# Optimization experiments

Hardware: AMD Instinct MI355X
Metric: run time of the kernel (lower is better)

Reference implementation:

```python
import jax, jax.numpy as jnp
import numpy as np

N_NODES = 50000
N_RAND_EDGES = 800000
N_GRAPHS = 64
IN_DIM, HID, HEADS = 1024, 64, 4
NEG_SLOPE = 0.2  # PyG GATConv default


def setup_inputs() -> dict:
    key = jax.random.key(0)
    ks = jax.random.split(key, 16)
    x = jax.random.normal(ks[0], (N_NODES, IN_DIM), dtype=jnp.float32)
    src = jax.random.randint(ks[1], (N_RAND_EDGES,), 0, N_NODES, dtype=jnp.int32)
    dst = jax.random.randint(ks[2], (N_RAND_EDGES,), 0, N_NODES, dtype=jnp.int32)
    loop = jnp.arange(N_NODES, dtype=jnp.int32)
    # PyG GATConv adds self-loops by default; bake them into edge_index.
    edge_index = jnp.stack([jnp.concatenate([src, loop]), jnp.concatenate([dst, loop])])
    batch = jnp.sort(jax.random.randint(ks[3], (N_NODES,), 0, N_GRAPHS, dtype=jnp.int32))
    s = 0.05
    W1 = jax.random.normal(ks[4], (IN_DIM, HEADS * HID), dtype=jnp.float32) * s
    att_src1 = jax.random.normal(ks[5], (HEADS, HID), dtype=jnp.float32) * s
    att_dst1 = jax.random.normal(ks[6], (HEADS, HID), dtype=jnp.float32) * s
    b1 = jnp.zeros((HEADS * HID,), dtype=jnp.float32)
    W2 = jax.random.normal(ks[7], (HEADS * HID, HID), dtype=jnp.float32) * s
    att_src2 = jax.random.normal(ks[8], (1, HID), dtype=jnp.float32) * s
    att_dst2 = jax.random.normal(ks[9], (1, HID), dtype=jnp.float32) * s
    b2 = jnp.zeros((HID,), dtype=jnp.float32)
    fc_w = jax.random.normal(ks[10], (HID, 2), dtype=jnp.float32) * s
    fc_b = jnp.zeros((2,), dtype=jnp.float32)
    return {"x": x, "edge_index": edge_index, "batch": batch,
            "W1": W1, "att_src1": att_src1, "att_dst1": att_dst1, "b1": b1,
            "W2": W2, "att_src2": att_src2, "att_dst2": att_dst2, "b2": b2,
            "fc_w": fc_w, "fc_b": fc_b}


def gat_conv(x, src, dst, W, a_src, a_dst, b):
    """PyG GATConv (eval mode, concat=True). x:[N,Fin] -> [N, H*C]."""
    N = x.shape[0]
    H, C = a_src.shape
    h = (x @ W).reshape(N, H, C)                      # [N,H,C]
    al_s = jnp.einsum('nhc,hc->nh', h, a_src)         # [N,H]
    al_d = jnp.einsum('nhc,hc->nh', h, a_dst)
    e = jax.nn.leaky_relu(al_s[src] + al_d[dst], NEG_SLOPE)   # [E,H]
    # segment-softmax over edges grouped by destination node
    m = jax.ops.segment_max(e, dst, num_segments=N)           # [N,H]
    w = jnp.exp(e - m[dst])
    denom = jax.ops.segment_sum(w, dst, num_segments=N)
    alpha = w / denom[dst]                                    # [E,H]
    msg = h[src] * alpha[:, :, None]                          # [E,H,C]
    out = jax.ops.segment_sum(msg, dst, num_segments=N)       # [N,H,C]
    return out.reshape(N, H * C) + b


def reference(x, edge_index, batch, W1, att_src1, att_dst1, b1,
              W2, att_src2, att_dst2, b2, fc_w, fc_b):
    src, dst = edge_index[0], edge_index[1]
    # dropout is identity in eval mode
    h = jax.nn.elu(gat_conv(x, src, dst, W1, att_src1, att_dst1, b1))
    h = jax.nn.elu(gat_conv(h, src, dst, W2, att_src2, att_dst2, b2))
    # global mean pool over graphs
    sums = jax.ops.segment_sum(h, batch, num_segments=N_GRAPHS)          # [G,HID]
    cnt = jax.ops.segment_sum(jnp.ones((h.shape[0],), h.dtype), batch,
                              num_segments=N_GRAPHS)
    pooled = sums / jnp.maximum(cnt, 1.0)[:, None]
    return pooled @ fc_w + fc_b                                          # [G,2]
```

## Files before the change

kernel.cpp:

```cpp
#include <hip/hip_runtime.h>
#include <hip/hip_bf16.h>

#define NNODES   50000
#define NGRAPHS  64
#define INDIM    1024
#define HIDC     64
#define HEADS1   4
#define F1       (HEADS1*HIDC)
#define NEG_SLOPE 0.2f

#define WS_COUNTS   0
#define WS_ZEROLEN  50000
#define WS_INDPTR   54208
#define WS_CURSOR   104256
#define WS_CSRSRC   154304
#define WS_CSRDST   1004304
#define WS_BSUM     1854304
#define WS_ALS1     1854368
#define WS_ALD1     2054368
#define WS_ALS2     2254368
#define WS_ALD2     2304368
#define WS_BP       2354368
#define WS_BP2      2485440
#define WS_H1B      2493632
#define WS_X2B      8893632
#define WS_H2B      15293632
#define WS_HFIN     16893632

typedef __attribute__((ext_vector_type(8))) short bf16x8;
typedef __attribute__((ext_vector_type(4))) float f32x4;

__device__ __forceinline__ ushort f2bf(float f) {
    union { float f; uint u; } v; v.f = f;
    uint r = v.u + 0x7fff + ((v.u >> 16) & 1);
    return (ushort)(r >> 16);
}
__device__ __forceinline__ float bf2f(ushort u) {
    union { uint u; float f; } v; v.u = (uint)u << 16; return v.f;
}

__global__ void zero_kernel(float* p, int n) {
    int i = blockIdx.x * blockDim.x + threadIdx.x;
    if (i < n) p[i] = 0.0f;
}

__global__ void hist_kernel(const int* __restrict__ dst, int* __restrict__ counts, int E) {
    int i = blockIdx.x * blockDim.x + threadIdx.x;
    if (i < E) atomicAdd(&counts[dst[i]], 1);
}

__global__ __launch_bounds__(1024) void scan1_kernel(const int* __restrict__ counts,
                                                     int* __restrict__ indptr,
                                                     int* __restrict__ bsum, int N) {
    __shared__ int sm[1024];
    int b = blockIdx.x;
    int i = b * 1024 + (int)threadIdx.x;
    int v = (i < N) ? counts[i] : 0;
    sm[threadIdx.x] = v;
    __syncthreads();
    for (int off = 1; off < 1024; off <<= 1) {
        int t = (threadIdx.x >= (unsigned)off) ? sm[threadIdx.x - off] : 0;
        __syncthreads();
        sm[threadIdx.x] += t;
        __syncthreads();
    }
    if (i < N) indptr[i + 1] = sm[threadIdx.x];
    if (threadIdx.x == 1023) bsum[b] = sm[1023];
}

__global__ void scan2_kernel(int* __restrict__ bsum, int nb) {
    int lane = threadIdx.x;
    int v = (lane < nb) ? bsum[lane] : 0;
    int orig = v;
    #pragma unroll
    for (int off = 1; off < 64; off <<= 1) {
        int t = __shfl_up(v, off, 64);
        if (lane >= off) v += t;
    }
    if (lane < nb) bsum[lane] = v - orig;
}

__global__ __launch_bounds__(1024) void scan3_kernel(const int* __restrict__ counts,
                                                     int* __restrict__ indptr,
                                                     int* __restrict__ cursor,
                                                     const int* __restrict__ bsum, int N) {
    int i = blockIdx.x * 1024 + (int)threadIdx.x;
    if (i == 0) indptr[0] = 0;
    if (i < N) {
        int incl = indptr[i + 1] + bsum[blockIdx.x];
        indptr[i + 1] = incl;
        cursor[i] = incl - counts[i];
    }
}

__global__ void fill_kernel(const int* __restrict__ src, const int* __restrict__ dst,
                            int* __restrict__ cursor, int* __restrict__ csr_src,
                            int* __restrict__ csr_dst, int E) {
    int i = blockIdx.x * blockDim.x + threadIdx.x;
    if (i < E) {
        int d = dst[i];
        int pos = atomicAdd(&cursor[d], 1);
        csr_src[pos] = src[i];
        csr_dst[pos] = d;
    }
}

__global__ void pack_w1(const float* __restrict__ W, ushort* __restrict__ Bp) {
    int o = blockIdx.x * blockDim.x + threadIdx.x;
    int j = o & 7;
    int lane = (o >> 3) & 63;
    int kchunk = (o >> 9) & 31;
    int ntile = o >> 14;
    int k = kchunk * 32 + (lane >> 4) * 8 + j;
    int n = ntile * 16 + (lane & 15);
    Bp[o] = f2bf(W[k * 256 + n]);
}

__global__ void pack_w2(const float* __restrict__ W, ushort* __restrict__ Bp) {
    int o = blockIdx.x * blockDim.x + threadIdx.x;
    int j = o & 7;
    int lane = (o >> 3) & 63;
    int kchunk = (o >> 9) & 7;
    int ntile = o >> 12;
    int k = kchunk * 32 + (lane >> 4) * 8 + j;
    int n = ntile * 16 + (lane & 15);
    Bp[o] = f2bf(W[k * 64 + n]);
}

__global__ __launch_bounds__(256) void gemm1_mfma(const float* __restrict__ A,
                                                  const ushort* __restrict__ Bp,
                                                  ushort* __restrict__ C,
                                                  const float* __restrict__ asrc,
                                                  const float* __restrict__ adst,
                                                  float* __restrict__ als,
                                                  float* __restrict__ ald,
                                                  int M) {
    __shared__ __align__(16) ushort Atile[2][128 * 32];
    const int K = 1024, N = 256;
    int tid = threadIdx.x;
    int lane = tid & 63;
    int w = tid >> 6;
    int wm = w >> 1, wn = w & 1;
    int m0 = blockIdx.x * 128;

    const float* srow[4];
    int soff[4];
    #pragma unroll
    for (int l = 0; l < 4; ++l) {
        int slot = l * 256 + tid;
        int m = slot >> 3, hc = slot & 7;
        int c = hc >> 1;
        int row = m0 + m; if (row >= M) row = M - 1;
        srow[l] = A + (size_t)row * K + hc * 4;
        soff[l] = (m * 4 + (c ^ ((m >> 1) & 3))) * 8 + (hc & 1) * 4;
    }
    int afrag_off[4];
    #pragma unroll
    for (int mt = 0; mt < 4; ++mt) {
        int r = wm * 64 + mt * 16 + (lane & 15);
        int cq = lane >> 4;
        afrag_off[mt] = (r * 4 + (cq ^ ((r >> 1) & 3))) * 8;
    }
    const ushort* bbase[8];
    #pragma unroll
    for (int nt = 0; nt < 8; ++nt) {
        int ntile = wn * 8 + nt;
        bbase[nt] = Bp + ((size_t)(ntile * 32) * 64 + lane) * 8;
    }

    f32x4 acc[4][8] = {};
    float4 v[4];
    #pragma unroll
    for (int l = 0; l < 4; ++l) v[l] = *(const float4*)(srow[l]);

    for (int kc = 0; kc < 32; ++kc) {
        ushort* At = Atile[kc & 1];
        #pragma unroll
        for (int l = 0; l < 4; ++l) {
            ushort4 b;
            b.x = f2bf(v[l].x); b.y = f2bf(v[l].y);
            b.z = f2bf(v[l].z); b.w = f2bf(v[l].w);
            *(ushort4*)&At[soff[l]] = b;
        }
        __syncthreads();
        if (kc < 31) {
            #pragma unroll
            for (int l = 0; l < 4; ++l)
                v[l] = *(const float4*)(srow[l] + (kc + 1) * 32);
        }
        bf16x8 afr[4];
        #pragma unroll
        for (int mt = 0; mt < 4; ++mt)
            afr[mt] = *(const bf16x8*)&At[afrag_off[mt]];
        #pragma unroll
        for (int nt = 0; nt < 8; ++nt) {
            bf16x8 bfr = *(const bf16x8*)(bbase[nt] + (size_t)kc * 64 * 8);
            #pragma unroll
            for (int mt = 0; mt < 4; ++mt)
                acc[mt][nt] = __builtin_amdgcn_mfma_f32_16x16x32_bf16(afr[mt], bfr, acc[mt][nt], 0, 0, 0);
        }
    }

    float a_s[8], a_d[8];
    #pragma unroll
    for (int nt = 0; nt < 8; ++nt) {
        int col = wn * 128 + nt * 16 + (lane & 15);
        a_s[nt] = asrc[col];
        a_d[nt] = adst[col];
    }
    #pragma unroll
    for (int mt = 0; mt < 4; ++mt) {
        #pragma unroll
        for (int nt = 0; nt < 8; ++nt) {
            int col = wn * 128 + nt * 16 + (lane & 15);
            #pragma unroll
            for (int r = 0; r < 4; ++r) {
                int row = m0 + wm * 64 + mt * 16 + (lane >> 4) * 4 + r;
                if (row < M) C[(size_t)row * N + col] = f2bf(acc[mt][nt][r]);
            }
        }
        #pragma unroll
        for (int hg = 0; hg < 2; ++hg) {
            int head = wn * 2 + hg;
            #pragma unroll
            for (int r = 0; r < 4; ++r) {
                int row = m0 + wm * 64 + mt * 16 + (lane >> 4) * 4 + r;
                float s = 0.f, d = 0.f;
                #pragma unroll
                for (int q = 0; q < 4; ++q) {
                    float c = acc[mt][4 * hg + q][r];
                    s = fmaf(c, a_s[4 * hg + q], s);
                    d = fmaf(c, a_d[4 * hg + q], d);
                }
                #pragma unroll
                for (int off = 1; off < 16; off <<= 1) {
                    s += __shfl_xor(s, off, 64);
                    d += __shfl_xor(d, off, 64);
                }
                if ((lane & 15) == 0 && row < M) {
                    als[row * 4 + head] = s;
                    ald[row * 4 + head] = d;
                }
            }
        }
    }
}

__global__ __launch_bounds__(256) void gemm2_mfma(const ushort* __restrict__ Ab,
                                                  const ushort* __restrict__ Bp,
                                                  ushort* __restrict__ C,
                                                  const float* __restrict__ asrc,
                                                  const float* __restrict__ adst,
                                                  float* __restrict__ als,
                                                  float* __restrict__ ald,
                                                  int M) {
    int tid = threadIdx.x;
    int lane = tid & 63;
    int w = tid >> 6;
    int m0 = blockIdx.x * 128 + w * 32;

    f32x4 acc[2][4] = {};
    #pragma unroll 2
    for (int kc = 0; kc < 8; ++kc) {
        bf16x8 afr[2];
        #pragma unroll
        for (int mt = 0; mt < 2; ++mt) {
            int r = m0 + mt * 16 + (lane & 15);
            if (r >= M) r = M - 1;
            afr[mt] = *(const bf16x8*)&Ab[(size_t)r * 256 + kc * 32 + (lane >> 4) * 8];
        }
        #pragma unroll
        for (int nt = 0; nt < 4; ++nt) {
            bf16x8 bfr = *(const bf16x8*)&Bp[((nt * 8 + kc) * 64 + lane) * 8];
            acc[0][nt] = __builtin_amdgcn_mfma_f32_16x16x32_bf16(afr[0], bfr, acc[0][nt], 0, 0, 0);
            acc[1][nt] = __builtin_amdgcn_mfma_f32_16x16x32_bf16(afr[1], bfr, acc[1][nt], 0, 0, 0);
        }
    }
    float a_s[4], a_d[4];
    #pragma unroll
    for (int nt = 0; nt < 4; ++nt) {
        a_s[nt] = asrc[nt * 16 + (lane & 15)];
        a_d[nt] = adst[nt * 16 + (lane & 15)];
    }
    #pragma unroll
    for (int mt = 0; mt < 2; ++mt) {
        #pragma unroll
        for (int nt = 0; nt < 4; ++nt) {
            int col = nt * 16 + (lane & 15);
            #pragma unroll
            for (int r = 0; r < 4; ++r) {
                int row = m0 + mt * 16 + (lane >> 4) * 4 + r;
                if (row < M) C[(size_t)row * 64 + col] = f2bf(acc[mt][nt][r]);
            }
        }
        #pragma unroll
        for (int r = 0; r < 4; ++r) {
            int row = m0 + mt * 16 + (lane >> 4) * 4 + r;
            float s = 0.f, d = 0.f;
            #pragma unroll
            for (int nt = 0; nt < 4; ++nt) {
                float c = acc[mt][nt][r];
                s = fmaf(c, a_s[nt], s);
                d = fmaf(c, a_d[nt], d);
            }
            #pragma unroll
            for (int off = 1; off < 16; off <<= 1) {
                s += __shfl_xor(s, off, 64);
                d += __shfl_xor(d, off, 64);
            }
            if ((lane & 15) == 0 && row < M) {
                als[row] = s;
                ald[row] = d;
            }
        }
    }
}

__device__ __forceinline__ float wave_reduce_sum(float v) {
    #pragma unroll
    for (int off = 32; off > 0; off >>= 1) v += __shfl_xor(v, off, 64);
    return v;
}

__device__ __forceinline__ float edge_w(float e) {
    e = (e > 0.f) ? e : NEG_SLOPE * e;
    return __expf(e);
}

__global__ __launch_bounds__(256) void agg1_kernel(const ushort* __restrict__ h,
                                                   const float* __restrict__ als,
                                                   const float* __restrict__ ald,
                                                   const int* __restrict__ indptr,
                                                   const int* __restrict__ csr_src,
                                                   const float* __restrict__ bias,
                                                   ushort* __restrict__ out, int N) {
    __shared__ float4 lacc[4][64];
    __shared__ float  lden[4][64];
    int n = blockIdx.x;
    int lane = threadIdx.x & 63;
    int wv = threadIdx.x >> 6;
    int hd = lane >> 4;
    int beg = indptr[n], end = indptr[n + 1];
    float ald_h = ald[n * 4 + hd];
    float4 acc = make_float4(0.f, 0.f, 0.f, 0.f);
    float den = 0.f;
    int p = beg + wv;
    for (; p + 4 < end; p += 8) {
        int s0 = csr_src[p], s1 = csr_src[p + 4];
        float w0 = edge_w(als[s0 * 4 + hd] + ald_h);
        float w1 = edge_w(als[s1 * 4 + hd] + ald_h);
        ushort4 a0 = *(const ushort4*)&h[(size_t)s0 * 256 + lane * 4];
        ushort4 a1 = *(const ushort4*)&h[(size_t)s1 * 256 + lane * 4];
        acc.x = fmaf(w0, bf2f(a0.x), fmaf(w1, bf2f(a1.x), acc.x));
        acc.y = fmaf(w0, bf2f(a0.y), fmaf(w1, bf2f(a1.y), acc.y));
        acc.z = fmaf(w0, bf2f(a0.z), fmaf(w1, bf2f(a1.z), acc.z));
        acc.w = fmaf(w0, bf2f(a0.w), fmaf(w1, bf2f(a1.w), acc.w));
        den += w0 + w1;
    }
    if (p < end) {
        int s0 = csr_src[p];
        float w0 = edge_w(als[s0 * 4 + hd] + ald_h);
        ushort4 a0 = *(const ushort4*)&h[(size_t)s0 * 256 + lane * 4];
        acc.x = fmaf(w0, bf2f(a0.x), acc.x);
        acc.y = fmaf(w0, bf2f(a0.y), acc.y);
        acc.z = fmaf(w0, bf2f(a0.z), acc.z);
        acc.w = fmaf(w0, bf2f(a0.w), acc.w);
        den += w0;
    }
    lacc[wv][lane] = acc;
    lden[wv][lane] = den;
    __syncthreads();
    if (wv == 0) {
        float4 a = lacc[0][lane];
        float4 a1 = lacc[1][lane], a2 = lacc[2][lane], a3 = lacc[3][lane];
        a.x += a1.x + a2.x + a3.x;
        a.y += a1.y + a2.y + a3.y;
        a.z += a1.z + a2.z + a3.z;
        a.w += a1.w + a2.w + a3.w;
        float d = lden[0][lane] + lden[1][lane] + lden[2][lane] + lden[3][lane];
        float4 bv = *(const float4*)&bias[lane * 4];
        float inv = 1.0f / d;
        float o0 = a.x * inv + bv.x, o1 = a.y * inv + bv.y;
        float o2 = a.z * inv + bv.z, o3 = a.w * inv + bv.w;
        o0 = (o0 > 0.f) ? o0 : (__expf(o0) - 1.0f);
        o1 = (o1 > 0.f) ? o1 : (__expf(o1) - 1.0f);
        o2 = (o2 > 0.f) ? o2 : (__expf(o2) - 1.0f);
        o3 = (o3 > 0.f) ? o3 : (__expf(o3) - 1.0f);
        ushort4 ob; ob.x = f2bf(o0); ob.y = f2bf(o1); ob.z = f2bf(o2); ob.w = f2bf(o3);
        *(ushort4*)&out[(size_t)n * 256 + lane * 4] = ob;
    }
}

__global__ __launch_bounds__(256) void agg2_kernel(const ushort* __restrict__ h,
                                                   const float* __restrict__ als,
                                                   const float* __restrict__ ald,
                                                   const int* __restrict__ indptr,
                                                   const int* __restrict__ csr_src,
                                                   const float* __restrict__ bias,
                                                   float* __restrict__ out, int N) {
    __shared__ float2 lacc[8][32];
    __shared__ float  lden[8][32];
    int n = blockIdx.x;
    int lane = threadIdx.x & 63;
    int wv = threadIdx.x >> 6;
    int sl = wv * 2 + (lane >> 5);
    int l32 = lane & 31;
    int beg = indptr[n], end = indptr[n + 1];
    float ald_n = ald[n];
    float2 acc = make_float2(0.f, 0.f);
    float den = 0.f;
    for (int p = beg + sl; p < end; p += 8) {
        int s = csr_src[p];
        float wt = edge_w(als[s] + ald_n);
        ushort2 hv = *(const ushort2*)&h[(size_t)s * 64 + l32 * 2];
        acc.x = fmaf(wt, bf2f(hv.x), acc.x);
        acc.y = fmaf(wt, bf2f(hv.y), acc.y);
        den += wt;
    }
    lacc[sl][l32] = acc;
    lden[sl][l32] = den;
    __syncthreads();
    if (threadIdx.x < 32) {
        int c = threadIdx.x;
        float2 a = make_float2(0.f, 0.f);
        float d = 0.f;
        #pragma unroll
        for (int s = 0; s < 8; ++s) {
            a.x += lacc[s][c].x; a.y += lacc[s][c].y;
            d += lden[s][c];
        }
        float inv = 1.0f / d;
        float o0 = a.x * inv + bias[c * 2];
        float o1 = a.y * inv + bias[c * 2 + 1];
        o0 = (o0 > 0.f) ? o0 : (__expf(o0) - 1.0f);
        o1 = (o1 > 0.f) ? o1 : (__expf(o1) - 1.0f);
        *(float2*)&out[(size_t)n * 64 + c * 2] = make_float2(o0, o1);
    }
}

__global__ __launch_bounds__(256) void pool_fc_kernel(const float* __restrict__ hfin,
                                                      const int* __restrict__ batch,
                                                      const float* __restrict__ fc_w,
                                                      const float* __restrict__ fc_b,
                                                      float* __restrict__ out, int N) {
    __shared__ float lacc[4][64];
    int g = blockIdx.x;
    int beg, end;
    {
        int lo = 0, hi = N;
        while (lo < hi) { int mid = (lo + hi) >> 1; if (batch[mid] < g) lo = mid + 1; else hi = mid; }
        beg = lo;
        lo = beg; hi = N;
        while (lo < hi) { int mid = (lo + hi) >> 1; if (batch[mid] < g + 1) lo = mid + 1; else hi = mid; }
        end = lo;
    }
    int lane = threadIdx.x & 63;
    int wv = threadIdx.x >> 6;
    float acc = 0.f;
    for (int n = beg + wv; n < end; n += 4)
        acc += hfin[(size_t)n * 64 + lane];
    lacc[wv][lane] = acc;
    __syncthreads();
    if (wv == 0) {
        float s = lacc[0][lane] + lacc[1][lane] + lacc[2][lane] + lacc[3][lane];
        float cnt = fmaxf((float)(end - beg), 1.0f);
        float pooled = s / cnt;
        float p0 = wave_reduce_sum(pooled * fc_w[lane * 2 + 0]);
        float p1 = wave_reduce_sum(pooled * fc_w[lane * 2 + 1]);
        if (lane == 0) {
            out[g * 2 + 0] = p0 + fc_b[0];
            out[g * 2 + 1] = p1 + fc_b[1];
        }
    }
}

extern "C" void kernel_launch(void* const* d_in, const int* in_sizes, int n_in,
                              void* d_out, int out_size, void* d_ws, size_t ws_size,
                              hipStream_t stream) {
    const float* x      = (const float*)d_in[0];
    const int*   ei     = (const int*)d_in[1];
    const int*   batch  = (const int*)d_in[2];
    const float* W1     = (const float*)d_in[3];
    const float* asrc1  = (const float*)d_in[4];
    const float* adst1  = (const float*)d_in[5];
    const float* b1     = (const float*)d_in[6];
    const float* W2     = (const float*)d_in[7];
    const float* asrc2  = (const float*)d_in[8];
    const float* adst2  = (const float*)d_in[9];
    const float* b2     = (const float*)d_in[10];
    const float* fc_w   = (const float*)d_in[11];
    const float* fc_b   = (const float*)d_in[12];
    float* out          = (float*)d_out;

    const int N = in_sizes[2];
    const int E = in_sizes[1] / 2;
    const int* src = ei;
    const int* dst = ei + E;

    float* ws = (float*)d_ws;
    int*    counts  = (int*)(ws + WS_COUNTS);
    int*    indptr  = (int*)(ws + WS_INDPTR);
    int*    cursor  = (int*)(ws + WS_CURSOR);
    int*    csr_src = (int*)(ws + WS_CSRSRC);
    int*    csr_dst = (int*)(ws + WS_CSRDST);
    int*    bsum    = (int*)(ws + WS_BSUM);
    float*  al_s1   = ws + WS_ALS1;
    float*  al_d1   = ws + WS_ALD1;
    float*  al_s2   = ws + WS_ALS2;
    float*  al_d2   = ws + WS_ALD2;
    ushort* bp      = (ushort*)(ws + WS_BP);
    ushort* bp2     = (ushort*)(ws + WS_BP2);
    ushort* h1b     = (ushort*)(ws + WS_H1B);
    ushort* x2b     = (ushort*)(ws + WS_X2B);
    ushort* h2b     = (ushort*)(ws + WS_H2B);
    float*  hfin    = ws + WS_HFIN;

    const int nb = (N + 1023) / 1024;

    zero_kernel<<<(WS_ZEROLEN + 255) / 256, 256, 0, stream>>>(ws, WS_ZEROLEN);
    pack_w1<<<(INDIM * F1) / 256, 256, 0, stream>>>(W1, bp);
    pack_w2<<<(F1 * HIDC) / 256, 256, 0, stream>>>(W2, bp2);
    hist_kernel<<<(E + 255) / 256, 256, 0, stream>>>(dst, counts, E);
    scan1_kernel<<<nb, 1024, 0, stream>>>(counts, indptr, bsum, N);
    scan2_kernel<<<1, 64, 0, stream>>>(bsum, nb);
    scan3_kernel<<<nb, 1024, 0, stream>>>(counts, indptr, cursor, bsum, N);
    fill_kernel<<<(E + 255) / 256, 256, 0, stream>>>(src, dst, cursor, csr_src, csr_dst, E);
    gemm1_mfma<<<(N + 127) / 128, 256, 0, stream>>>(
        x, bp, h1b, asrc1, adst1, al_s1, al_d1, N);
    agg1_kernel<<<N, 256, 0, stream>>>(h1b, al_s1, al_d1, indptr, csr_src, b1, x2b, N);
    gemm2_mfma<<<(N + 127) / 128, 256, 0, stream>>>(
        x2b, bp2, h2b, asrc2, adst2, al_s2, al_d2, N);
    agg2_kernel<<<N, 256, 0, stream>>>(h2b, al_s2, al_d2, indptr, csr_src, b2, hfin, N);
    pool_fc_kernel<<<NGRAPHS, 256, 0, stream>>>(hfin, batch, fc_w, fc_b, out, N);
}
```

Measured before the change: 638.5 us.

## Assign one wave per node in aggregation with LDS-staged edge weights; fuse prep kernels

The aggregation kernels now give each destination node to a single wave (agg1) or half-wave (agg2) instead of a whole block. This removes the cross-wave LDS reduction and __syncthreads, and cuts the grid from N blocks to N/4 and N/8. Each wave loads up to 64 (or 32) edge sources cooperatively, computes the per-head softmax weights once, and stages them in LDS so the gather loop does not recompute exp per lane. The zeroing and the two weight-packing kernels are merged into one launch, and the unused csr_dst write in fill_kernel is dropped. The trade-off is less parallelism per node for high-degree nodes and a serial per-wave edge loop.

Measured after the change: 575.9 us. -9.8%, faster.

```diff
diff --git a/kernel.cpp b/kernel.cpp
--- a/kernel.cpp
+++ b/kernel.cpp
@@ -39,9 +39,33 @@
     union { uint u; float f; } v; v.u = (uint)u << 16; return v.f;
 }
 
-__global__ void zero_kernel(float* p, int n) {
-    int i = blockIdx.x * blockDim.x + threadIdx.x;
-    if (i < n) p[i] = 0.0f;
+__global__ void prep_kernel(const float* __restrict__ W1, const float* __restrict__ W2,
+                            ushort* __restrict__ Bp1, ushort* __restrict__ Bp2,
+                            int* __restrict__ counts) {
+    int b = blockIdx.x;
+    int tid = threadIdx.x;
+    if (b < 1024) {
+        int o = b * 256 + tid;
+        int j = o & 7;
+        int lane = (o >> 3) & 63;
+        int kchunk = (o >> 9) & 31;
+        int ntile = o >> 14;
+        int k = kchunk * 32 + (lane >> 4) * 8 + j;
+        int n = ntile * 16 + (lane & 15);
+        Bp1[o] = f2bf(W1[k * 256 + n]);
+    } else if (b < 1088) {
+        int o = (b - 1024) * 256 + tid;
+        int j = o & 7;
+        int lane = (o >> 3) & 63;
+        int kchunk = (o >> 9) & 7;
+        int ntile = o >> 12;
+        int k = kchunk * 32 + (lane >> 4) * 8 + j;
+        int n = ntile * 16 + (lane & 15);
+        Bp2[o] = f2bf(W2[k * 64 + n]);
+    } else {
+        int i = (b - 1088) * 256 + tid;
+        if (i < NNODES) counts[i] = 0;
+    }
 }
 
 __global__ void hist_kernel(const int* __restrict__ dst, int* __restrict__ counts, int E) {
@@ -94,37 +118,13 @@
 }
 
 __global__ void fill_kernel(const int* __restrict__ src, const int* __restrict__ dst,
-                            int* __restrict__ cursor, int* __restrict__ csr_src,
-                            int* __restrict__ csr_dst, int E) {
+                            int* __restrict__ cursor, int* __restrict__ csr_src, int E) {
     int i = blockIdx.x * blockDim.x + threadIdx.x;
     if (i < E) {
         int d = dst[i];
         int pos = atomicAdd(&cursor[d], 1);
         csr_src[pos] = src[i];
-        csr_dst[pos] = d;
-    }
-}
-
-__global__ void pack_w1(const float* __restrict__ W, ushort* __restrict__ Bp) {
-    int o = blockIdx.x * blockDim.x + threadIdx.x;
-    int j = o & 7;
-    int lane = (o >> 3) & 63;
-    int kchunk = (o >> 9) & 31;
-    int ntile = o >> 14;
-    int k = kchunk * 32 + (lane >> 4) * 8 + j;
-    int n = ntile * 16 + (lane & 15);
-    Bp[o] = f2bf(W[k * 256 + n]);
-}
-
-__global__ void pack_w2(const float* __restrict__ W, ushort* __restrict__ Bp) {
-    int o = blockIdx.x * blockDim.x + threadIdx.x;
-    int j = o & 7;
-    int lane = (o >> 3) & 63;
-    int kchunk = (o >> 9) & 7;
-    int ntile = o >> 12;
-    int k = kchunk * 32 + (lane >> 4) * 8 + j;
-    int n = ntile * 16 + (lane & 15);
-    Bp[o] = f2bf(W[k * 64 + n]);
+    }
 }
 
 __global__ __launch_bounds__(256) void gemm1_mfma(const float* __restrict__ A,
@@ -334,61 +334,53 @@
                                                    const int* __restrict__ csr_src,
                                                    const float* __restrict__ bias,
                                                    ushort* __restrict__ out, int N) {
-    __shared__ float4 lacc[4][64];
-    __shared__ float  lden[4][64];
-    int n = blockIdx.x;
+    __shared__ int   s_s[4][64];
+    __shared__ float s_w[4][64][4];
+    int wv   = threadIdx.x >> 6;
     int lane = threadIdx.x & 63;
-    int wv = threadIdx.x >> 6;
+    int n = blockIdx.x * 4 + wv;
+    if (n >= N) return;
     int hd = lane >> 4;
     int beg = indptr[n], end = indptr[n + 1];
-    float ald_h = ald[n * 4 + hd];
+    float4 aldv = *(const float4*)&ald[n * 4];
+
     float4 acc = make_float4(0.f, 0.f, 0.f, 0.f);
     float den = 0.f;
-    int p = beg + wv;
-    for (; p + 4 < end; p += 8) {
-        int s0 = csr_src[p], s1 = csr_src[p + 4];
-        float w0 = edge_w(als[s0 * 4 + hd] + ald_h);
-        float w1 = edge_w(als[s1 * 4 + hd] + ald_h);
-        ushort4 a0 = *(const ushort4*)&h[(size_t)s0 * 256 + lane * 4];
-        ushort4 a1 = *(const ushort4*)&h[(size_t)s1 * 256 + lane * 4];
-        acc.x = fmaf(w0, bf2f(a0.x), fmaf(w1, bf2f(a1.x), acc.x));
-        acc.y = fmaf(w0, bf2f(a0.y), fmaf(w1, bf2f(a1.y), acc.y));
-        acc.z = fmaf(w0, bf2f(a0.z), fmaf(w1, bf2f(a1.z), acc.z));
-        acc.w = fmaf(w0, bf2f(a0.w), fmaf(w1, bf2f(a1.w), acc.w));
-        den += w0 + w1;
-    }
-    if (p < end) {
-        int s0 = csr_src[p];
-        float w0 = edge_w(als[s0 * 4 + hd] + ald_h);
-        ushort4 a0 = *(const ushort4*)&h[(size_t)s0 * 256 + lane * 4];
-        acc.x = fmaf(w0, bf2f(a0.x), acc.x);
-        acc.y = fmaf(w0, bf2f(a0.y), acc.y);
-        acc.z = fmaf(w0, bf2f(a0.z), acc.z);
-        acc.w = fmaf(w0, bf2f(a0.w), acc.w);
-        den += w0;
-    }
-    lacc[wv][lane] = acc;
-    lden[wv][lane] = den;
-    __syncthreads();
-    if (wv == 0) {
-        float4 a = lacc[0][lane];
-        float4 a1 = lacc[1][lane], a2 = lacc[2][lane], a3 = lacc[3][lane];
-        a.x += a1.x + a2.x + a3.x;
-        a.y += a1.y + a2.y + a3.y;
-        a.z += a1.z + a2.z + a3.z;
-        a.w += a1.w + a2.w + a3.w;
-        float d = lden[0][lane] + lden[1][lane] + lden[2][lane] + lden[3][lane];
-        float4 bv = *(const float4*)&bias[lane * 4];
-        float inv = 1.0f / d;
-        float o0 = a.x * inv + bv.x, o1 = a.y * inv + bv.y;
-        float o2 = a.z * inv + bv.z, o3 = a.w * inv + bv.w;
-        o0 = (o0 > 0.f) ? o0 : (__expf(o0) - 1.0f);
-        o1 = (o1 > 0.f) ? o1 : (__expf(o1) - 1.0f);
-        o2 = (o2 > 0.f) ? o2 : (__expf(o2) - 1.0f);
-        o3 = (o3 > 0.f) ? o3 : (__expf(o3) - 1.0f);
-        ushort4 ob; ob.x = f2bf(o0); ob.y = f2bf(o1); ob.z = f2bf(o2); ob.w = f2bf(o3);
-        *(ushort4*)&out[(size_t)n * 256 + lane * 4] = ob;
-    }
+
+    for (int base = beg; base < end; base += 64) {
+        int cnt = end - base; if (cnt > 64) cnt = 64;
+        if (lane < cnt) {
+            int s = csr_src[base + lane];
+            s_s[wv][lane] = s;
+            float4 av = *(const float4*)&als[s * 4];
+            s_w[wv][lane][0] = edge_w(av.x + aldv.x);
+            s_w[wv][lane][1] = edge_w(av.y + aldv.y);
+            s_w[wv][lane][2] = edge_w(av.z + aldv.z);
+            s_w[wv][lane][3] = edge_w(av.w + aldv.w);
+        }
+        #pragma unroll 4
+        for (int e = 0; e < cnt; ++e) {
+            int s = s_s[wv][e];
+            float wt = s_w[wv][e][hd];
+            ushort4 a = *(const ushort4*)&h[(size_t)s * 256 + lane * 4];
+            acc.x = fmaf(wt, bf2f(a.x), acc.x);
+            acc.y = fmaf(wt, bf2f(a.y), acc.y);
+            acc.z = fmaf(wt, bf2f(a.z), acc.z);
+            acc.w = fmaf(wt, bf2f(a.w), acc.w);
+            den += wt;
+        }
+    }
+
+    float inv = 1.0f / den;
+    float4 bv = *(const float4*)&bias[lane * 4];
+    float o0 = acc.x * inv + bv.x, o1 = acc.y * inv + bv.y;
+    float o2 = acc.z * inv + bv.z, o3 = acc.w * inv + bv.w;
+    o0 = (o0 > 0.f) ? o0 : (__expf(o0) - 1.0f);
+    o1 = (o1 > 0.f) ? o1 : (__expf(o1) - 1.0f);
+    o2 = (o2 > 0.f) ? o2 : (__expf(o2) - 1.0f);
+    o3 = (o3 > 0.f) ? o3 : (__expf(o3) - 1.0f);
+    ushort4 ob; ob.x = f2bf(o0); ob.y = f2bf(o1); ob.z = f2bf(o2); ob.w = f2bf(o3);
+    *(ushort4*)&out[(size_t)n * 256 + lane * 4] = ob;
 }
 
 __global__ __launch_bounds__(256) void agg2_kernel(const ushort* __restrict__ h,
@@ -398,44 +390,43 @@
                                                    const int* __restrict__ csr_src,
                                                    const float* __restrict__ bias,
                                                    float* __restrict__ out, int N) {
-    __shared__ float2 lacc[8][32];
-    __shared__ float  lden[8][32];
-    int n = blockIdx.x;
-    int lane = threadIdx.x & 63;
-    int wv = threadIdx.x >> 6;
-    int sl = wv * 2 + (lane >> 5);
-    int l32 = lane & 31;
+    __shared__ int   s_s[8][32];
+    __shared__ float s_w[8][32];
+    int tid = threadIdx.x;
+    int sl  = tid >> 5;
+    int l32 = tid & 31;
+    int n = blockIdx.x * 8 + sl;
+    if (n >= N) return;
     int beg = indptr[n], end = indptr[n + 1];
     float ald_n = ald[n];
+
     float2 acc = make_float2(0.f, 0.f);
     float den = 0.f;
-    for (int p = beg + sl; p < end; p += 8) {
-        int s = csr_src[p];
-        float wt = edge_w(als[s] + ald_n);
-        ushort2 hv = *(const ushort2*)&h[(size_t)s * 64 + l32 * 2];
-        acc.x = fmaf(wt, bf2f(hv.x), acc.x);
-        acc.y = fmaf(wt, bf2f(hv.y), acc.y);
-        den += wt;
-    }
-    lacc[sl][l32] = acc;
-    lden[sl][l32] = den;
-    __syncthreads();
-    if (threadIdx.x < 32) {
-        int c = threadIdx.x;
-        float2 a = make_float2(0.f, 0.f);
-        float d = 0.f;
-        #pragma unroll
-        for (int s = 0; s < 8; ++s) {
-            a.x += lacc[s][c].x; a.y += lacc[s][c].y;
-            d += lden[s][c];
-        }
-        float inv = 1.0f / d;
-        float o0 = a.x * inv + bias[c * 2];
-        float o1 = a.y * inv + bias[c * 2 + 1];
-        o0 = (o0 > 0.f) ? o0 : (__expf(o0) - 1.0f);
-        o1 = (o1 > 0.f) ? o1 : (__expf(o1) - 1.0f);
-        *(float2*)&out[(size_t)n * 64 + c * 2] = make_float2(o0, o1);
-    }
+
+    for (int base = beg; base < end; base += 32) {
+        int cnt = end - base; if (cnt > 32) cnt = 32;
+        if (l32 < cnt) {
+            int s = csr_src[base + l32];
+            s_s[sl][l32] = s;
+            s_w[sl][l32] = edge_w(als[s] + ald_n);
+        }
+        #pragma unroll 4
+        for (int e = 0; e < cnt; ++e) {
+            int s = s_s[sl][e];
+            float wt = s_w[sl][e];
+            ushort2 hv = *(const ushort2*)&h[(size_t)s * 64 + l32 * 2];
+            acc.x = fmaf(wt, bf2f(hv.x), acc.x);
+            acc.y = fmaf(wt, bf2f(hv.y), acc.y);
+            den += wt;
+        }
+    }
+
+    float inv = 1.0f / den;
+    float o0 = acc.x * inv + bias[l32 * 2];
+    float o1 = acc.y * inv + bias[l32 * 2 + 1];
+    o0 = (o0 > 0.f) ? o0 : (__expf(o0) - 1.0f);
+    o1 = (o1 > 0.f) ? o1 : (__expf(o1) - 1.0f);
+    *(float2*)&out[(size_t)n * 64 + l32 * 2] = make_float2(o0, o1);
 }
 
 __global__ __launch_bounds__(256) void pool_fc_kernel(const float* __restrict__ hfin,
@@ -502,7 +493,6 @@
     int*    indptr  = (int*)(ws + WS_INDPTR);
     int*    cursor  = (int*)(ws + WS_CURSOR);
     int*    csr_src = (int*)(ws + WS_CSRSRC);
-    int*    csr_dst = (int*)(ws + WS_CSRDST);
     int*    bsum    = (int*)(ws + WS_BSUM);
     float*  al_s1   = ws + WS_ALS1;
     float*  al_d1   = ws + WS_ALD1;
@@ -517,19 +507,17 @@
 
     const int nb = (N + 1023) / 1024;
 
-    zero_kernel<<<(WS_ZEROLEN + 255) / 256, 256, 0, stream>>>(ws, WS_ZEROLEN);
-    pack_w1<<<(INDIM * F1) / 256, 256, 0, stream>>>(W1, bp);
-    pack_w2<<<(F1 * HIDC) / 256, 256, 0, stream>>>(W2, bp2);
+    prep_kernel<<<1284, 256, 0, stream>>>(W1, W2, bp, bp2, counts);
     hist_kernel<<<(E + 255) / 256, 256, 0, stream>>>(dst, counts, E);
     scan1_kernel<<<nb, 1024, 0, stream>>>(counts, indptr, bsum, N);
     scan2_kernel<<<1, 64, 0, stream>>>(bsum, nb);
     scan3_kernel<<<nb, 1024, 0, stream>>>(counts, indptr, cursor, bsum, N);
-    fill_kernel<<<(E + 255) / 256, 256, 0, stream>>>(src, dst, cursor, csr_src, csr_dst, E);
+    fill_kernel<<<(E + 255) / 256, 256, 0, stream>>>(src, dst, cursor, csr_src, E);
     gemm1_mfma<<<(N + 127) / 128, 256, 0, stream>>>(
         x, bp, h1b, asrc1, adst1, al_s1, al_d1, N);
-    agg1_kernel<<<N, 256, 0, stream>>>(h1b, al_s1, al_d1, indptr, csr_src, b1, x2b, N);
+    agg1_kernel<<<(N + 3) / 4, 256, 0, stream>>>(h1b, al_s1, al_d1, indptr, csr_src, b1, x2b, N);
     gemm2_mfma<<<(N + 127) / 128, 256, 0, stream>>>(
         x2b, bp2, h2b, asrc2, adst2, al_s2, al_d2, N);
-    agg2_kernel<<<N, 256, 0, stream>>>(h2b, al_s2, al_d2, indptr, csr_src, b2, hfin, N);
+    agg2_kernel<<<(N + 7) / 8, 256, 0, stream>>>(h2b, al_s2, al_d2, indptr, csr_src, b2, hfin, N);
     pool_fc_kernel<<<NGRAPHS, 256, 0, stream>>>(hfin, batch, fc_w, fc_b, out, N);
 }
```
